# Kernel tuning notes

Measured on AMD Instinct MI355X. Metric: run time of the kernel, lower is better.

## Reference

```python
import jax, jax.numpy as jnp
import numpy as np

N_NODES = 50000
IN_CH = 128
HID = 128
N_EDGES = 800000


def _glorot(key, shape):
    fan_in, fan_out = shape[0], shape[1]
    lim = (6.0 / (fan_in + fan_out)) ** 0.5
    return jax.random.uniform(key, shape, jnp.float32, -lim, lim)


def setup_inputs() -> dict:
    key = jax.random.key(0)
    ks = jax.random.split(key, 8)
    x = jax.random.normal(ks[0], (N_NODES, IN_CH), jnp.float32)
    edge_index = jax.random.randint(ks[1], (2, N_EDGES), 0, N_NODES, jnp.int64)
    return {
        "x": x,
        "edge_index": edge_index,
        # SAGEConv1: lin_l (with bias) applied to mean-aggregated neighbors,
        # lin_r (no bias) applied to root features (PyG defaults, mean aggr)
        "W1l": _glorot(ks[2], (IN_CH, HID)),
        "b1l": jnp.zeros((HID,), jnp.float32),
        "W1r": _glorot(ks[3], (IN_CH, HID)),
        # SAGEConv2
        "W2l": _glorot(ks[4], (HID, HID)),
        "b2l": jnp.zeros((HID,), jnp.float32),
        "W2r": _glorot(ks[5], (HID, HID)),
        # final Linear(hidden, 1)
        "Wout": _glorot(ks[6], (HID, 1)),
        "bout": jnp.zeros((1,), jnp.float32),
    }


def _sage_conv(x, src, dst, Wl, bl, Wr, n_nodes):
    # gather source features along edges, mean-reduce into destinations
    msgs = x[src]                                                # [E, D]
    sums = jax.ops.segment_sum(msgs, dst, num_segments=n_nodes)  # [N, D]
    cnt = jax.ops.segment_sum(jnp.ones((src.shape[0], 1), x.dtype), dst,
                              num_segments=n_nodes)              # [N, 1]
    agg = sums / jnp.maximum(cnt, 1.0)
    return agg @ Wl + bl + x @ Wr


def reference(x, edge_index, W1l, b1l, W1r, W2l, b2l, W2r, Wout, bout):
    src, dst = edge_index[0], edge_index[1]
    n = x.shape[0]
    h = jax.nn.relu(_sage_conv(x, src, dst, W1l, b1l, W1r, n))
    h = jax.nn.relu(_sage_conv(h, src, dst, W2l, b2l, W2r, n))
    return (h @ Wout + bout).squeeze(-1)  # [N]
```

## Files before the change

kernel.cpp:

```cpp
#include <hip/hip_runtime.h>

#define D 128
#define LSTR 132
#define CAP 3072
#define NBLK 256

typedef __attribute__((ext_vector_type(8))) short short8;
typedef __attribute__((ext_vector_type(4))) float f32x4;

static __device__ __forceinline__ unsigned short f2bf(float f) {
    unsigned u = __float_as_uint(f);
    return (unsigned short)((u + 0x7fffu + ((u >> 16) & 1u)) >> 16);
}
static __device__ __forceinline__ float b2f(unsigned short u) {
    return __uint_as_float(((unsigned)u) << 16);
}


__global__ __launch_bounds__(256) void prep_hist_kernel(
    const float* __restrict__ x, const float* __restrict__ W1l,
    const float* __restrict__ W1r, const float* __restrict__ W2l,
    const float* __restrict__ W2r, unsigned* __restrict__ xb2,
    unsigned short* __restrict__ Bt1, unsigned short* __restrict__ Bt2,
    int NX2, const int* __restrict__ dst, int E, int nbins,
    unsigned* __restrict__ G) {
    const int t = threadIdx.x;
    if (blockIdx.x < NBLK) {
        __shared__ int h[2048];
        for (int i = t; i < nbins; i += 256) h[i] = 0;
        __syncthreads();
        const int per = (E + NBLK - 1) / NBLK;
        const int lo = blockIdx.x * per;
        const int hi = min(lo + per, E);
        for (int i = lo + t; i < hi; i += 256) atomicAdd(&h[dst[i] >> 5], 1);
        __syncthreads();
        for (int i = t; i < nbins; i += 256)
            G[(size_t)i * NBLK + blockIdx.x] = (unsigned)h[i];
        return;
    }
    const int i = (blockIdx.x - NBLK) * 256 + t;
    if (i < NX2) {
        const float2 v = *(const float2*)(x + 2 * (size_t)i);
        xb2[i] = (unsigned)f2bf(v.x) | ((unsigned)f2bf(v.y) << 16);
    } else if (i < NX2 + 2 * 32768) {
        const int j = i - NX2;
        const int which = j >> 15;
        const int jj = j & 32767;
        const int n = jj >> 8;
        const int k = jj & 255;
        const float* Wl = which ? W2l : W1l;
        const float* Wr = which ? W2r : W1r;
        const float w = (k < 128) ? Wl[k * 128 + n] : Wr[(k - 128) * 128 + n];
        (which ? Bt2 : Bt1)[jj] = f2bf(w);
    }
}

__global__ __launch_bounds__(256) void scanB_kernel(unsigned* __restrict__ G,
                                                    int nbins,
                                                    int* __restrict__ tot) {
    const int wave = threadIdx.x >> 6;
    const int lane = threadIdx.x & 63;
    const int bin = blockIdx.x * 4 + wave;
    if (bin >= nbins) return;
    unsigned* p = G + (size_t)bin * NBLK + lane * 4;
    uint4 v = *(uint4*)p;
    const unsigned s = v.x + v.y + v.z + v.w;
    unsigned sc = s;
#pragma unroll
    for (int off = 1; off < 64; off <<= 1) {
        const unsigned u = (unsigned)__shfl_up((int)sc, off, 64);
        if (lane >= off) sc += u;
    }
    const unsigned excl = sc - s;
    uint4 w;
    w.x = excl;
    w.y = excl + v.x;
    w.z = excl + v.x + v.y;
    w.w = excl + v.x + v.y + v.z;
    *(uint4*)p = w;
    if (lane == 63) tot[bin] = (int)(excl + s);
}

__global__ __launch_bounds__(1024) void scanC_kernel(
    const int* __restrict__ tot, int nbins, int* __restrict__ tile_base) {
    __shared__ int part[1024];
    const int t = threadIdx.x;
    const int chunk = (nbins + 1023) >> 10;
    const int lo = min(t * chunk, nbins);
    const int hi = min(lo + chunk, nbins);
    int s = 0;
    for (int i = lo; i < hi; ++i) s += tot[i];
    part[t] = s;
    __syncthreads();
    for (int off = 1; off < 1024; off <<= 1) {
        int add = (t >= off) ? part[t - off] : 0;
        __syncthreads();
        part[t] += add;
        __syncthreads();
    }
    int excl = (t == 0) ? 0 : part[t - 1];
    for (int i = lo; i < hi; ++i) {
        tile_base[i] = excl;
        excl += tot[i];
    }
    if (t == 1023) tile_base[nbins] = part[1023];
}

__global__ __launch_bounds__(256) void fillB_kernel(
    const int* __restrict__ src, const int* __restrict__ dst, int E,
    const unsigned* __restrict__ G, const int* __restrict__ tile_base,
    unsigned* __restrict__ csr, int nbins) {
    __shared__ int rank[2048];
    __shared__ int base[2048];
    const int t = threadIdx.x;
    for (int i = t; i < nbins; i += 256) {
        rank[i] = 0;
        base[i] = tile_base[i] + (int)G[(size_t)i * NBLK + blockIdx.x];
    }
    __syncthreads();
    const int per = (E + NBLK - 1) / NBLK;
    const int lo = blockIdx.x * per;
    const int hi = min(lo + per, E);
    for (int i = lo + t; i < hi; i += 256) {
        const int d = dst[i];
        const int bin = d >> 5;
        const int r = atomicAdd(&rank[bin], 1);
        csr[base[bin] + r] = (unsigned)src[i] | ((unsigned)d << 16);
    }
}

__global__ __launch_bounds__(256) void sortT_kernel(unsigned* __restrict__ csr,
                                                    const int* __restrict__
                                                        tile_base,
                                                    float* __restrict__ invL_g,
                                                    int N) {
    __shared__ unsigned sortedE[CAP];
    __shared__ int rowcnt[32];
    __shared__ int rowofs[32];
    const int b = blockIdx.x;
    const int i0 = b * 32;
    const int t = threadIdx.x;
    const int rs0 = tile_base[b];
    const int re0 = tile_base[b + 1];
    const int nE = re0 - rs0;

    if (t < 32) rowcnt[t] = 0;
    __syncthreads();
    for (int i = t; i < nE; i += 256)
        atomicAdd(&rowcnt[(csr[rs0 + i] >> 16) & 31], 1);
    __syncthreads();
    if (t < 32) {
        const int v = rowcnt[t];
        if (i0 + t < N) invL_g[i0 + t] = 1.0f / fmaxf((float)v, 1.0f);
        int s = v;
#pragma unroll
        for (int off = 1; off < 32; off <<= 1) {
            const int u = __shfl_up(s, off, 32);
            if ((t & 31) >= off) s += u;
        }
        rowofs[t] = s - v;
    }
    __syncthreads();
    if (nE <= CAP) {
        for (int i = t; i < nE; i += 256) {
            const unsigned p = csr[rs0 + i];
            const int k = atomicAdd(&rowofs[(p >> 16) & 31], 1);
            sortedE[k] = p;
        }
        __syncthreads();
        for (int i = t; i < nE; i += 256) csr[rs0 + i] = sortedE[i];
    }
}

template <bool HEAD>
__global__ __launch_bounds__(256) void sage_kernel(
    const unsigned short* __restrict__ xb, const unsigned* __restrict__ csr,
    const int* __restrict__ tile_base, const float* __restrict__ invL_g,
    const unsigned short* __restrict__ Bt,
    const float* __restrict__ bl, const float* __restrict__ Wout,
    const float* __restrict__ bout, unsigned short* __restrict__ hb_out,
    float* __restrict__ out, int N) {
    __shared__ float aggL[32 * LSTR];
    __shared__ float invL[32];
    __shared__ float redH[64];

    const int b = blockIdx.x;
    const int i0 = b * 32;
    const int t = threadIdx.x;
    const int g = t >> 5;
    const int l = t & 31;
    const int c4 = l << 2;

    for (int i = t; i < 32 * LSTR; i += 256) aggL[i] = 0.f;
    if (t < 32) invL[t] = (i0 + t < N) ? invL_g[i0 + t] : 1.0f;
    __syncthreads();

    const int rs0 = tile_base[b];
    const int re0 = tile_base[b + 1];
    const int nE = re0 - rs0;
    int e = rs0 + ((nE * g) >> 3);
    const int ee = rs0 + ((nE * (g + 1)) >> 3);

    float4 acc = make_float4(0.f, 0.f, 0.f, 0.f);
    int cur = (e < ee) ? (int)(csr[e] >> 16) - i0 : -1;

    auto load4 = [&](unsigned p) -> float4 {
        const ushort4 u =
            *(const ushort4*)(xb + (size_t)(p & 0xffffu) * D + c4);
        float4 v;
        v.x = b2f(u.x); v.y = b2f(u.y); v.z = b2f(u.z); v.w = b2f(u.w);
        return v;
    };
    auto step = [&](unsigned p, const float4& v) {
        const int r = (int)(p >> 16) - i0;
        if (r != cur) {
            float* q = aggL + cur * LSTR + c4;
            atomicAdd(q + 0, acc.x);
            atomicAdd(q + 1, acc.y);
            atomicAdd(q + 2, acc.z);
            atomicAdd(q + 3, acc.w);
            acc = make_float4(0.f, 0.f, 0.f, 0.f);
            cur = r;
        }
        acc.x += v.x; acc.y += v.y; acc.z += v.z; acc.w += v.w;
    };

    while (e + 8 <= ee) {
        const unsigned p0 = csr[e + 0], p1 = csr[e + 1];
        const unsigned p2 = csr[e + 2], p3 = csr[e + 3];
        const unsigned p4 = csr[e + 4], p5 = csr[e + 5];
        const unsigned p6 = csr[e + 6], p7 = csr[e + 7];
        const float4 v0 = load4(p0), v1 = load4(p1), v2 = load4(p2),
                     v3 = load4(p3), v4 = load4(p4), v5 = load4(p5),
                     v6 = load4(p6), v7 = load4(p7);
        step(p0, v0); step(p1, v1); step(p2, v2); step(p3, v3);
        step(p4, v4); step(p5, v5); step(p6, v6); step(p7, v7);
        e += 8;
    }
    while (e < ee) {
        const unsigned p = csr[e];
        step(p, load4(p));
        ++e;
    }
    if (cur >= 0) {
        float* q = aggL + cur * LSTR + c4;
        atomicAdd(q + 0, acc.x);
        atomicAdd(q + 1, acc.y);
        atomicAdd(q + 2, acc.z);
        atomicAdd(q + 3, acc.w);
    }
    __syncthreads();

    const int wave = t >> 6;
    const int lane = t & 63;
    const int ln = lane & 15;
    const int quad = lane >> 4;
    const int mtile = wave & 1;
    const int nt0 = (wave >> 1) * 4;
    const int mrow = mtile * 16 + ln;
    const int gmr = i0 + mrow;
    const float inv = invL[mrow];

    f32x4 acc4[4] = {f32x4{0.f, 0.f, 0.f, 0.f}, f32x4{0.f, 0.f, 0.f, 0.f},
                     f32x4{0.f, 0.f, 0.f, 0.f}, f32x4{0.f, 0.f, 0.f, 0.f}};

#pragma unroll
    for (int s = 0; s < 4; ++s) {
        const int kb = s * 32 + quad * 8;
        const float* ap = aggL + mrow * LSTR + kb;
        const float4 fa = *(const float4*)ap;
        const float4 fb = *(const float4*)(ap + 4);
        const short8 aA = {(short)f2bf(fa.x * inv), (short)f2bf(fa.y * inv),
                           (short)f2bf(fa.z * inv), (short)f2bf(fa.w * inv),
                           (short)f2bf(fb.x * inv), (short)f2bf(fb.y * inv),
                           (short)f2bf(fb.z * inv), (short)f2bf(fb.w * inv)};
        short8 aX = {0, 0, 0, 0, 0, 0, 0, 0};
        if (gmr < N) aX = *(const short8*)(xb + (size_t)gmr * D + kb);
#pragma unroll
        for (int nt = 0; nt < 4; ++nt) {
            const int n = (nt0 + nt) * 16 + ln;
            const short8 b1 = *(const short8*)(Bt + n * 256 + kb);
            const short8 b2 = *(const short8*)(Bt + n * 256 + 128 + kb);
            acc4[nt] = __builtin_amdgcn_mfma_f32_16x16x32_bf16(aA, b1, acc4[nt],
                                                               0, 0, 0);
            acc4[nt] = __builtin_amdgcn_mfma_f32_16x16x32_bf16(aX, b2, acc4[nt],
                                                               0, 0, 0);
        }
    }

    float biasv[4], woutv[4];
#pragma unroll
    for (int nt = 0; nt < 4; ++nt) {
        const int col = (nt0 + nt) * 16 + ln;
        biasv[nt] = bl[col];
        if (HEAD) woutv[nt] = Wout[col];
    }

    if (!HEAD) {
#pragma unroll
        for (int r = 0; r < 4; ++r) {
            const int gr = i0 + mtile * 16 + quad * 4 + r;
            if (gr < N) {
#pragma unroll
                for (int nt = 0; nt < 4; ++nt) {
                    const int col = (nt0 + nt) * 16 + ln;
                    const float v = fmaxf(acc4[nt][r] + biasv[nt], 0.f);
                    hb_out[(size_t)gr * D + col] = f2bf(v);
                }
            }
        }
    } else {
        const float b0 = bout[0];
#pragma unroll
        for (int r = 0; r < 4; ++r) {
            const int row = mtile * 16 + quad * 4 + r;
            float p = 0.f;
#pragma unroll
            for (int nt = 0; nt < 4; ++nt) {
                const float v = fmaxf(acc4[nt][r] + biasv[nt], 0.f);
                p += v * woutv[nt];
            }
            p += __shfl_xor(p, 1);
            p += __shfl_xor(p, 2);
            p += __shfl_xor(p, 4);
            p += __shfl_xor(p, 8);
            if (ln == 0) redH[row * 2 + (wave >> 1)] = p;
        }
        __syncthreads();
        if (t < 32) {
            const int gr = i0 + t;
            if (gr < N) out[gr] = redH[t * 2] + redH[t * 2 + 1] + b0;
        }
    }
}

extern "C" void kernel_launch(void* const* d_in, const int* in_sizes, int n_in,
                              void* d_out, int out_size, void* d_ws,
                              size_t ws_size, hipStream_t stream) {
    const float* x = (const float*)d_in[0];
    const int* ei = (const int*)d_in[1];
    const float* W1l = (const float*)d_in[2];
    const float* b1l = (const float*)d_in[3];
    const float* W1r = (const float*)d_in[4];
    const float* W2l = (const float*)d_in[5];
    const float* b2l = (const float*)d_in[6];
    const float* W2r = (const float*)d_in[7];
    const float* Wout = (const float*)d_in[8];
    const float* bout = (const float*)d_in[9];

    const int N = in_sizes[0] / D;
    const int E = in_sizes[1] / 2;
    const int* src = ei;
    const int* dst = ei + E;

    const int nbins = (N + 31) / 32;
    const size_t Npad = (size_t)((N + 255) & ~255);
    const size_t Epad = (size_t)((E + 255) & ~255);

    int* tot = (int*)d_ws;
    int* tile_base = tot + 2048;
    float* invL_g = (float*)(tile_base + 2052);
    unsigned* G = (unsigned*)(invL_g + Npad);
    unsigned* csr = G + (size_t)2048 * NBLK;
    unsigned short* xb = (unsigned short*)(csr + Epad);
    unsigned short* hb = xb + (size_t)N * D;
    unsigned short* Bt1 = hb + (size_t)N * D;
    unsigned short* Bt2 = Bt1 + 128 * 256;
    float* out = (float*)d_out;

    const int NX2 = N * D / 2;
    const int prep_blocks = (NX2 + 2 * 32768 + 255) / 256;

    prep_hist_kernel<<<NBLK + prep_blocks, 256, 0, stream>>>(
        x, W1l, W1r, W2l, W2r, (unsigned*)xb, Bt1, Bt2, NX2, dst, E, nbins, G);
    scanB_kernel<<<(nbins + 3) / 4, 256, 0, stream>>>(G, nbins, tot);
    scanC_kernel<<<1, 1024, 0, stream>>>(tot, nbins, tile_base);
    fillB_kernel<<<NBLK, 256, 0, stream>>>(src, dst, E, G, tile_base, csr,
                                           nbins);
    sortT_kernel<<<nbins, 256, 0, stream>>>(csr, tile_base, invL_g, N);

    sage_kernel<false><<<nbins, 256, 0, stream>>>(
        xb, csr, tile_base, invL_g, Bt1, b1l, nullptr, nullptr, hb, nullptr, N);
    sage_kernel<true><<<nbins, 256, 0, stream>>>(
        hb, csr, tile_base, invL_g, Bt2, b2l, Wout, bout, nullptr, out, N);
}
```

Before: 258.4 us.

## Replace global bin scan kernel with atomic allocation and deepen gather unroll

Removes the single-block scanC kernel. Each bin instead claims its output range with an atomicAdd on a global counter, and bins store start/end pairs, so bin segments are no longer in bin order but stay contiguous. This saves one kernel launch and a serial single-block scan. The aggregation loop in sage_kernel also now issues 16 gathers per iteration instead of 8, to raise memory-level parallelism at the cost of more registers.

```diff
diff --git a/kernel.cpp b/kernel.cpp
--- a/kernel.cpp
+++ b/kernel.cpp
@@ -23,7 +23,7 @@
     const float* __restrict__ W2r, unsigned* __restrict__ xb2,
     unsigned short* __restrict__ Bt1, unsigned short* __restrict__ Bt2,
     int NX2, const int* __restrict__ dst, int E, int nbins,
-    unsigned* __restrict__ G) {
+    unsigned* __restrict__ G, int* __restrict__ gctr) {
     const int t = threadIdx.x;
     if (blockIdx.x < NBLK) {
         __shared__ int h[2048];
@@ -38,6 +38,7 @@
             G[(size_t)i * NBLK + blockIdx.x] = (unsigned)h[i];
         return;
     }
+    if (blockIdx.x == NBLK && t == 0) *gctr = 0;
     const int i = (blockIdx.x - NBLK) * 256 + t;
     if (i < NX2) {
         const float2 v = *(const float2*)(x + 2 * (size_t)i);
@@ -57,7 +58,8 @@
 
 __global__ __launch_bounds__(256) void scanB_kernel(unsigned* __restrict__ G,
                                                     int nbins,
-                                                    int* __restrict__ tot) {
+                                                    int* __restrict__ tile_base,
+                                                    int* __restrict__ gctr) {
     const int wave = threadIdx.x >> 6;
     const int lane = threadIdx.x & 63;
     const int bin = blockIdx.x * 4 + wave;
@@ -78,32 +80,14 @@
     w.z = excl + v.x + v.y;
     w.w = excl + v.x + v.y + v.z;
     *(uint4*)p = w;
-    if (lane == 63) tot[bin] = (int)(excl + s);
-}
-
-__global__ __launch_bounds__(1024) void scanC_kernel(
-    const int* __restrict__ tot, int nbins, int* __restrict__ tile_base) {
-    __shared__ int part[1024];
-    const int t = threadIdx.x;
-    const int chunk = (nbins + 1023) >> 10;
-    const int lo = min(t * chunk, nbins);
-    const int hi = min(lo + chunk, nbins);
-    int s = 0;
-    for (int i = lo; i < hi; ++i) s += tot[i];
-    part[t] = s;
-    __syncthreads();
-    for (int off = 1; off < 1024; off <<= 1) {
-        int add = (t >= off) ? part[t - off] : 0;
-        __syncthreads();
-        part[t] += add;
-        __syncthreads();
-    }
-    int excl = (t == 0) ? 0 : part[t - 1];
-    for (int i = lo; i < hi; ++i) {
-        tile_base[i] = excl;
-        excl += tot[i];
-    }
-    if (t == 1023) tile_base[nbins] = part[1023];
+    const unsigned tot = __shfl((int)(excl + s), 63, 64);
+    int base = 0;
+    if (lane == 63) base = atomicAdd(gctr, (int)tot);
+    base = __shfl(base, 63, 64);
+    if (lane == 0) {
+        tile_base[2 * bin] = base;
+        tile_base[2 * bin + 1] = base + (int)tot;
+    }
 }
 
 __global__ __launch_bounds__(256) void fillB_kernel(
@@ -115,7 +99,7 @@
     const int t = threadIdx.x;
     for (int i = t; i < nbins; i += 256) {
         rank[i] = 0;
-        base[i] = tile_base[i] + (int)G[(size_t)i * NBLK + blockIdx.x];
+        base[i] = tile_base[2 * i] + (int)G[(size_t)i * NBLK + blockIdx.x];
     }
     __syncthreads();
     const int per = (E + NBLK - 1) / NBLK;
@@ -140,8 +124,8 @@
     const int b = blockIdx.x;
     const int i0 = b * 32;
     const int t = threadIdx.x;
-    const int rs0 = tile_base[b];
-    const int re0 = tile_base[b + 1];
+    const int rs0 = tile_base[2 * b];
+    const int re0 = tile_base[2 * b + 1];
     const int nE = re0 - rs0;
 
     if (t < 32) rowcnt[t] = 0;
@@ -195,8 +179,8 @@
     if (t < 32) invL[t] = (i0 + t < N) ? invL_g[i0 + t] : 1.0f;
     __syncthreads();
 
-    const int rs0 = tile_base[b];
-    const int re0 = tile_base[b + 1];
+    const int rs0 = tile_base[2 * b];
+    const int re0 = tile_base[2 * b + 1];
     const int nE = re0 - rs0;
     int e = rs0 + ((nE * g) >> 3);
     const int ee = rs0 + ((nE * (g + 1)) >> 3);
@@ -225,16 +209,26 @@
         acc.x += v.x; acc.y += v.y; acc.z += v.z; acc.w += v.w;
     };
 
-    while (e + 8 <= ee) {
-        const unsigned p0 = csr[e + 0], p1 = csr[e + 1];
-        const unsigned p2 = csr[e + 2], p3 = csr[e + 3];
-        const unsigned p4 = csr[e + 4], p5 = csr[e + 5];
-        const unsigned p6 = csr[e + 6], p7 = csr[e + 7];
-        const float4 v0 = load4(p0), v1 = load4(p1), v2 = load4(p2),
-                     v3 = load4(p3), v4 = load4(p4), v5 = load4(p5),
-                     v6 = load4(p6), v7 = load4(p7);
-        step(p0, v0); step(p1, v1); step(p2, v2); step(p3, v3);
-        step(p4, v4); step(p5, v5); step(p6, v6); step(p7, v7);
+    while (e + 16 <= ee) {
+        unsigned p[16];
+        float4 v[16];
+#pragma unroll
+        for (int j = 0; j < 16; ++j) p[j] = csr[e + j];
+#pragma unroll
+        for (int j = 0; j < 16; ++j) v[j] = load4(p[j]);
+#pragma unroll
+        for (int j = 0; j < 16; ++j) step(p[j], v[j]);
+        e += 16;
+    }
+    if (e + 8 <= ee) {
+        unsigned p[8];
+        float4 v[8];
+#pragma unroll
+        for (int j = 0; j < 8; ++j) p[j] = csr[e + j];
+#pragma unroll
+        for (int j = 0; j < 8; ++j) v[j] = load4(p[j]);
+#pragma unroll
+        for (int j = 0; j < 8; ++j) step(p[j], v[j]);
         e += 8;
     }
     while (e < ee) {
@@ -357,9 +351,9 @@
     const size_t Npad = (size_t)((N + 255) & ~255);
     const size_t Epad = (size_t)((E + 255) & ~255);
 
-    int* tot = (int*)d_ws;
-    int* tile_base = tot + 2048;
-    float* invL_g = (float*)(tile_base + 2052);
+    int* tile_base = (int*)d_ws;
+    int* gctr = tile_base + 4096;
+    float* invL_g = (float*)(gctr + 4);
     unsigned* G = (unsigned*)(invL_g + Npad);
     unsigned* csr = G + (size_t)2048 * NBLK;
     unsigned short* xb = (unsigned short*)(csr + Epad);
@@ -372,9 +366,10 @@
     const int prep_blocks = (NX2 + 2 * 32768 + 255) / 256;
 
     prep_hist_kernel<<<NBLK + prep_blocks, 256, 0, stream>>>(
-        x, W1l, W1r, W2l, W2r, (unsigned*)xb, Bt1, Bt2, NX2, dst, E, nbins, G);
-    scanB_kernel<<<(nbins + 3) / 4, 256, 0, stream>>>(G, nbins, tot);
-    scanC_kernel<<<1, 1024, 0, stream>>>(tot, nbins, tile_base);
+        x, W1l, W1r, W2l, W2r, (unsigned*)xb, Bt1, Bt2, NX2, dst, E, nbins, G,
+        gctr);
+    scanB_kernel<<<(nbins + 3) / 4, 256, 0, stream>>>(G, nbins, tile_base,
+                                                      gctr);
     fillB_kernel<<<NBLK, 256, 0, stream>>>(src, dst, E, G, tile_base, csr,
                                            nbins);
     sortT_kernel<<<nbins, 256, 0, stream>>>(csr, tile_base, invL_g, N);
```

Result: slower. 277.3 us (+7.3%).
